# Optimization experiments

Measured on AMD Instinct MI355X. Metric: run time of the kernel, lower is better.

The kernel has to match this reference:

```python
import jax, jax.numpy as jnp
import numpy as np

ACT_BW = 8
PAR_BW = 4
EPS = 1e-8

def fake_quant(t, bw):
    # symmetric per-tensor fake quantization with dynamic absmax observer
    qmax = float(2 ** (bw - 1) - 1)
    scale = jnp.maximum(jnp.max(jnp.abs(t)) / qmax, EPS)
    q = jnp.clip(jnp.round(t / scale), -qmax, qmax) * scale
    # straight-through estimator (matches torch fake-quant backward)
    return t + jax.lax.stop_gradient(q - t)

def setup_inputs() -> dict:
    key = jax.random.key(0)
    k1, k2, k3 = jax.random.split(key, 3)
    tokens, d_in, d_out = 4096, 4096, 4096
    x = jax.random.normal(k1, (tokens, d_in), dtype=jnp.float32)
    # kaiming-uniform-ish init scale
    bound_w = 1.0 / np.sqrt(d_in)
    weight = jax.random.uniform(k2, (d_out, d_in), dtype=jnp.float32, minval=-bound_w, maxval=bound_w)
    b = jax.random.uniform(k3, (d_out,), dtype=jnp.float32, minval=-bound_w, maxval=bound_w)
    return {"x": x, "weight": weight, "b": b}

def reference(x, weight, b):
    # 1) requantize input activations (act_bitwidth)
    xq = fake_quant(x, ACT_BW)
    # 2) quantize weight (par_bitwidth), transpose [out,in] -> [in,out]
    wq = fake_quant(weight, PAR_BW).T
    # 3) quantize bias (act_bitwidth)
    bq = fake_quant(b, ACT_BW)
    # 4) AddMM: bias + x @ w^T, then requantize the output (multiplier's quantizer)
    out = bq + jnp.matmul(xq, wq)  # [tokens, out_features]
    return fake_quant(out, ACT_BW)
```

## Files before the change

kernel.cpp:

```cpp
#include <hip/hip_runtime.h>

#define NELEM (4096 * 4096)
#define KDIM 4096
#define NDIM 4096
#define DOUT 4096
#define EPSQ 1e-8f
#define STRIDE_MEM (2048 * 256)

typedef __attribute__((ext_vector_type(4))) int i32x4;

typedef __attribute__((address_space(3))) void lds_void;
typedef const __attribute__((address_space(1))) void gbl_void;

__device__ __forceinline__ void load_lds16(const void* g, void* l) {
    __builtin_amdgcn_global_load_lds((gbl_void*)g, (lds_void*)l, 16, 0, 0);
}

__device__ __forceinline__ float wave_max64(float v) {
#pragma unroll
    for (int off = 32; off > 0; off >>= 1)
        v = fmaxf(v, __shfl_down(v, off));
    return v;
}

__global__ __launch_bounds__(256) void absmax_xwb(
    const float4* __restrict__ x, const float4* __restrict__ w,
    const float* __restrict__ b, unsigned* __restrict__ amax)
{
    float mx = 0.f, mw = 0.f;
    int i = blockIdx.x * 256 + threadIdx.x;
#pragma unroll
    for (int it = 0; it < 8; ++it, i += STRIDE_MEM) {
        float4 a = x[i];
        float4 c = w[i];
        mx = fmaxf(mx, fmaxf(fmaxf(fabsf(a.x), fabsf(a.y)), fmaxf(fabsf(a.z), fabsf(a.w))));
        mw = fmaxf(mw, fmaxf(fmaxf(fabsf(c.x), fabsf(c.y)), fmaxf(fabsf(c.z), fabsf(c.w))));
    }
    float mb = 0.f;
    if (blockIdx.x == 0) {
#pragma unroll
        for (int t = 0; t < DOUT / 256; ++t)
            mb = fmaxf(mb, fabsf(b[t * 256 + threadIdx.x]));
    }

    mx = wave_max64(mx); mw = wave_max64(mw); mb = wave_max64(mb);
    __shared__ float red[3][4];
    const int wave = threadIdx.x >> 6, lane = threadIdx.x & 63;
    if (lane == 0) { red[0][wave] = mx; red[1][wave] = mw; red[2][wave] = mb; }
    __syncthreads();
    if (threadIdx.x == 0) {
        float r0 = fmaxf(fmaxf(red[0][0], red[0][1]), fmaxf(red[0][2], red[0][3]));
        float r1 = fmaxf(fmaxf(red[1][0], red[1][1]), fmaxf(red[1][2], red[1][3]));
        atomicMax(&amax[0], __float_as_uint(r0));
        atomicMax(&amax[1], __float_as_uint(r1));
        if (blockIdx.x == 0) {
            float r2 = fmaxf(fmaxf(red[2][0], red[2][1]), fmaxf(red[2][2], red[2][3]));
            atomicMax(&amax[2], __float_as_uint(r2));
        }
    }
}

__device__ __forceinline__ int pack4(float4 a, float s, float qmax) {
    int b0 = (int)fminf(fmaxf(rintf(a.x / s), -qmax), qmax);
    int b1 = (int)fminf(fmaxf(rintf(a.y / s), -qmax), qmax);
    int b2 = (int)fminf(fmaxf(rintf(a.z / s), -qmax), qmax);
    int b3 = (int)fminf(fmaxf(rintf(a.w / s), -qmax), qmax);
    return (b0 & 0xff) | ((b1 & 0xff) << 8) | ((b2 & 0xff) << 16) | (b3 << 24);
}

__global__ __launch_bounds__(256) void quant_xwb(
    const float4* __restrict__ x, const float4* __restrict__ w,
    const float* __restrict__ b, const unsigned* __restrict__ amax,
    int* __restrict__ qx, int* __restrict__ qw, float* __restrict__ bq)
{
    const float sx = fmaxf(__uint_as_float(amax[0]) / 127.0f, EPSQ);
    const float sw = fmaxf(__uint_as_float(amax[1]) / 7.0f, EPSQ);
    int i = blockIdx.x * 256 + threadIdx.x;
#pragma unroll
    for (int it = 0; it < 8; ++it, i += STRIDE_MEM) {
        qx[i] = pack4(x[i], sx, 127.f);
        qw[i] = pack4(w[i], sw, 7.f);
    }
    if (blockIdx.x == 0) {
        const float sb = fmaxf(__uint_as_float(amax[2]) / 127.0f, EPSQ);
#pragma unroll
        for (int t = 0; t < DOUT / 256; ++t) {
            int j = t * 256 + threadIdx.x;
            float q = fminf(fmaxf(rintf(b[j] / sb), -127.f), 127.f);
            bq[j] = q * sb;
        }
    }
}

__global__ __launch_bounds__(512, 2) void gemm_i8_8p(
    const char* __restrict__ qx,
    const char* __restrict__ qw,
    const float* __restrict__ bq,
    const unsigned* __restrict__ amax,
    float* __restrict__ out,
    unsigned* __restrict__ amax_out)
{
    constexpr int K = KDIM, N = NDIM;
    __shared__ char lds[131072];
    char* ldsA = lds;
    char* ldsB = lds + 65536;

    const int tid = threadIdx.x;
    const int wave = tid >> 6, lane = tid & 63;
    const int swz = (blockIdx.x & 7) * 32 + (blockIdx.x >> 3);
    const int bm = swz >> 4, bn = swz & 15;
    const int wm2 = wave >> 2;
    const int wn4 = wave & 3;

    const int sg16 = (((lane & 3) ^ ((lane >> 3) & 3)) << 4);
    const char* aG = qx + (size_t)(bm * 256 + wave * 16 + (lane >> 2)) * K + sg16;
    const char* bG = qw + (size_t)(bn * 256 + wave * 16 + (lane >> 2)) * K + sg16;

    const int frow = lane & 15;
    const int fks = (((lane >> 4) ^ ((frow >> 1) & 3)) << 4);
    const int aoff = (wm2 * 128 + frow) * 64 + fks;
    const int boff = (wn4 * 64 + frow) * 64 + fks;

    i32x4 acc[8][4] = {};

#define STAGE8(s) { const int p_ = (s) & 3;                                                  \
    load_lds16(aG + (size_t)(s) * 64,                  ldsA + p_ * 16384 + wave * 1024);     \
    load_lds16(aG + (size_t)128 * K + (size_t)(s) * 64, ldsA + p_ * 16384 + 8192 + wave * 1024); \
    load_lds16(bG + (size_t)(s) * 64,                  ldsB + p_ * 16384 + wave * 1024);     \
    load_lds16(bG + (size_t)128 * K + (size_t)(s) * 64, ldsB + p_ * 16384 + 8192 + wave * 1024); }

#define PHASE8(s, VMN, DO_ST) {                                                              \
    asm volatile("s_waitcnt vmcnt(%0)" :: "n"(VMN) : "memory");                              \
    __builtin_amdgcn_s_barrier();                                                            \
    __builtin_amdgcn_sched_barrier(0);                                                       \
    if (DO_ST) STAGE8((s) + 3);                                                              \
    const char* Ab = ldsA + ((s) & 3) * 16384 + aoff;                                        \
    const char* Bb = ldsB + ((s) & 3) * 16384 + boff;                                        \
    i32x4 af[8], bf[4];                                                                      \
    _Pragma("unroll") for (int mi = 0; mi < 8; ++mi)                                         \
        af[mi] = *(const i32x4*)(Ab + mi * 1024);                                            \
    _Pragma("unroll") for (int ni = 0; ni < 4; ++ni)                                         \
        bf[ni] = *(const i32x4*)(Bb + ni * 1024);                                            \
    __builtin_amdgcn_s_setprio(1);                                                           \
    _Pragma("unroll") for (int mi = 0; mi < 8; ++mi)                                         \
    _Pragma("unroll") for (int ni = 0; ni < 4; ++ni)                                         \
        acc[mi][ni] = __builtin_amdgcn_mfma_i32_16x16x64_i8(af[mi], bf[ni], acc[mi][ni], 0, 0, 0); \
    __builtin_amdgcn_s_setprio(0); }

    STAGE8(0); STAGE8(1); STAGE8(2);

    for (int s = 0; s < 61; ++s) PHASE8(s, 8, true);
    PHASE8(61, 8, false);
    PHASE8(62, 4, false);
    PHASE8(63, 0, false);

#undef PHASE8
#undef STAGE8

    const float sx = fmaxf(__uint_as_float(amax[0]) / 127.0f, EPSQ);
    const float sw = fmaxf(__uint_as_float(amax[1]) / 7.0f, EPSQ);
    const float s = sx * sw;
    const int col = lane & 15;
    const int rbase = (lane >> 4) * 4;
    float am = 0.f;
    float bqv[4];
#pragma unroll
    for (int ni = 0; ni < 4; ++ni) bqv[ni] = bq[bn * 256 + wn4 * 64 + ni * 16 + col];

#pragma unroll
    for (int mi = 0; mi < 8; ++mi) {
#pragma unroll
        for (int rr = 0; rr < 4; ++rr) {
            const int m = bm * 256 + wm2 * 128 + mi * 16 + rbase + rr;
            float* orow = out + (size_t)m * N + bn * 256 + wn4 * 64 + col;
#pragma unroll
            for (int ni = 0; ni < 4; ++ni) {
                float o = fmaf(s, (float)acc[mi][ni][rr], bqv[ni]);
                am = fmaxf(am, fabsf(o));
                orow[ni * 16] = o;
            }
        }
    }
    am = wave_max64(am);
    float* red = (float*)lds;
    if (lane == 0) red[wave] = am;
    __syncthreads();
    if (tid == 0) {
        float r = fmaxf(fmaxf(fmaxf(red[0], red[1]), fmaxf(red[2], red[3])),
                        fmaxf(fmaxf(red[4], red[5]), fmaxf(red[6], red[7])));
        atomicMax(amax_out, __float_as_uint(r));
    }
}

__global__ __launch_bounds__(256) void final_quant(
    float4* __restrict__ out, const unsigned* __restrict__ amax)
{
    const float so = fmaxf(__uint_as_float(amax[3]) / 127.0f, EPSQ);
    int i = blockIdx.x * 256 + threadIdx.x;
#pragma unroll
    for (int it = 0; it < 8; ++it, i += STRIDE_MEM) {
        float4 v = out[i];
        v.x = fminf(fmaxf(rintf(v.x / so), -127.f), 127.f) * so;
        v.y = fminf(fmaxf(rintf(v.y / so), -127.f), 127.f) * so;
        v.z = fminf(fmaxf(rintf(v.z / so), -127.f), 127.f) * so;
        v.w = fminf(fmaxf(rintf(v.w / so), -127.f), 127.f) * so;
        out[i] = v;
    }
}

extern "C" void kernel_launch(void* const* d_in, const int* in_sizes, int n_in,
                              void* d_out, int out_size, void* d_ws, size_t ws_size,
                              hipStream_t stream) {
    const float* x = (const float*)d_in[0];
    const float* w = (const float*)d_in[1];
    const float* b = (const float*)d_in[2];
    float* out = (float*)d_out;

    char* ws = (char*)d_ws;
    unsigned* amax = (unsigned*)ws;
    float* bq = (float*)(ws + 256);
    char* qx = (char*)(ws + 32768);
    char* qw = (char*)(ws + 32768 + (size_t)NELEM);

    hipMemsetAsync(amax, 0, 16, stream);
    hipLaunchKernelGGL(absmax_xwb, dim3(2048), dim3(256), 0, stream,
                       (const float4*)x, (const float4*)w, b, amax);
    hipLaunchKernelGGL(quant_xwb, dim3(2048), dim3(256), 0, stream,
                       (const float4*)x, (const float4*)w, b, amax,
                       (int*)qx, (int*)qw, bq);
    hipLaunchKernelGGL(gemm_i8_8p, dim3(256), dim3(512), 0, stream,
                       (const char*)qx, (const char*)qw, bq, amax, out, amax + 3);
    hipLaunchKernelGGL(final_quant, dim3(2048), dim3(256), 0, stream,
                       (float4*)out, amax);
}
```

Measured before the change: 280.4 us.

## Switch int8 GEMM to 32x32x32 MFMA and shard absmax atomics

```diff
diff --git a/kernel.cpp b/kernel.cpp
--- a/kernel.cpp
+++ b/kernel.cpp
@@ -8,6 +8,7 @@
 #define STRIDE_MEM (2048 * 256)
 
 typedef __attribute__((ext_vector_type(4))) int i32x4;
+typedef __attribute__((ext_vector_type(16))) int i32x16;
 
 typedef __attribute__((address_space(3))) void lds_void;
 typedef const __attribute__((address_space(1))) void gbl_void;
@@ -22,6 +23,7 @@
         v = fmaxf(v, __shfl_down(v, off));
     return v;
 }
+
 
 __global__ __launch_bounds__(256) void absmax_xwb(
     const float4* __restrict__ x, const float4* __restrict__ w,
@@ -51,13 +53,26 @@
     if (threadIdx.x == 0) {
         float r0 = fmaxf(fmaxf(red[0][0], red[0][1]), fmaxf(red[0][2], red[0][3]));
         float r1 = fmaxf(fmaxf(red[1][0], red[1][1]), fmaxf(red[1][2], red[1][3]));
-        atomicMax(&amax[0], __float_as_uint(r0));
-        atomicMax(&amax[1], __float_as_uint(r1));
+        const int sl = (blockIdx.x & 7) * 16;
+        atomicMax(&amax[sl], __float_as_uint(r0));
+        atomicMax(&amax[sl + 4], __float_as_uint(r1));
         if (blockIdx.x == 0) {
             float r2 = fmaxf(fmaxf(red[2][0], red[2][1]), fmaxf(red[2][2], red[2][3]));
-            atomicMax(&amax[2], __float_as_uint(r2));
+            atomicMax(&amax[128], __float_as_uint(r2));
         }
     }
+}
+
+__device__ __forceinline__ void load_scales(const unsigned* __restrict__ amax,
+                                            float& sx, float& sw) {
+    float sxm = 0.f, swm = 0.f;
+#pragma unroll
+    for (int j = 0; j < 8; ++j) {
+        sxm = fmaxf(sxm, __uint_as_float(amax[j * 16]));
+        swm = fmaxf(swm, __uint_as_float(amax[j * 16 + 4]));
+    }
+    sx = fmaxf(sxm / 127.0f, EPSQ);
+    sw = fmaxf(swm / 7.0f, EPSQ);
 }
 
 __device__ __forceinline__ int pack4(float4 a, float s, float qmax) {
@@ -73,8 +88,8 @@
     const float* __restrict__ b, const unsigned* __restrict__ amax,
     int* __restrict__ qx, int* __restrict__ qw, float* __restrict__ bq)
 {
-    const float sx = fmaxf(__uint_as_float(amax[0]) / 127.0f, EPSQ);
-    const float sw = fmaxf(__uint_as_float(amax[1]) / 7.0f, EPSQ);
+    float sx, sw;
+    load_scales(amax, sx, sw);
     int i = blockIdx.x * 256 + threadIdx.x;
 #pragma unroll
     for (int it = 0; it < 8; ++it, i += STRIDE_MEM) {
@@ -82,7 +97,7 @@
         qw[i] = pack4(w[i], sw, 7.f);
     }
     if (blockIdx.x == 0) {
-        const float sb = fmaxf(__uint_as_float(amax[2]) / 127.0f, EPSQ);
+        const float sb = fmaxf(__uint_as_float(amax[128]) / 127.0f, EPSQ);
 #pragma unroll
         for (int t = 0; t < DOUT / 256; ++t) {
             int j = t * 256 + threadIdx.x;
@@ -116,17 +131,18 @@
     const char* aG = qx + (size_t)(bm * 256 + wave * 16 + (lane >> 2)) * K + sg16;
     const char* bG = qw + (size_t)(bn * 256 + wave * 16 + (lane >> 2)) * K + sg16;
 
-    const int frow = lane & 15;
-    const int fks = (((lane >> 4) ^ ((frow >> 1) & 3)) << 4);
-    const int aoff = (wm2 * 128 + frow) * 64 + fks;
-    const int boff = (wn4 * 64 + frow) * 64 + fks;
-
-    i32x4 acc[8][4] = {};
+    const int l31 = lane & 31;
+    const int fks0 = ((((lane >> 5)) ^ ((lane >> 1) & 3)) << 4);
+    const int fks1 = ((((lane >> 5) | 2) ^ ((lane >> 1) & 3)) << 4);
+    const int aBase = wm2 * 8192 + l31 * 64;
+    const int bBase = (wn4 >> 1) * 8192 + (wn4 & 1) * 4096 + l31 * 64;
+
+    i32x16 acc[4][2] = {};
 
 #define STAGE8(s) { const int p_ = (s) & 3;                                                  \
-    load_lds16(aG + (size_t)(s) * 64,                  ldsA + p_ * 16384 + wave * 1024);     \
+    load_lds16(aG + (size_t)(s) * 64,                   ldsA + p_ * 16384 + wave * 1024);    \
     load_lds16(aG + (size_t)128 * K + (size_t)(s) * 64, ldsA + p_ * 16384 + 8192 + wave * 1024); \
-    load_lds16(bG + (size_t)(s) * 64,                  ldsB + p_ * 16384 + wave * 1024);     \
+    load_lds16(bG + (size_t)(s) * 64,                   ldsB + p_ * 16384 + wave * 1024);    \
     load_lds16(bG + (size_t)128 * K + (size_t)(s) * 64, ldsB + p_ * 16384 + 8192 + wave * 1024); }
 
 #define PHASE8(s, VMN, DO_ST) {                                                              \
@@ -134,17 +150,24 @@
     __builtin_amdgcn_s_barrier();                                                            \
     __builtin_amdgcn_sched_barrier(0);                                                       \
     if (DO_ST) STAGE8((s) + 3);                                                              \
-    const char* Ab = ldsA + ((s) & 3) * 16384 + aoff;                                        \
-    const char* Bb = ldsB + ((s) & 3) * 16384 + boff;                                        \
-    i32x4 af[8], bf[4];                                                                      \
-    _Pragma("unroll") for (int mi = 0; mi < 8; ++mi)                                         \
-        af[mi] = *(const i32x4*)(Ab + mi * 1024);                                            \
-    _Pragma("unroll") for (int ni = 0; ni < 4; ++ni)                                         \
-        bf[ni] = *(const i32x4*)(Bb + ni * 1024);                                            \
+    const char* Ab = ldsA + ((s) & 3) * 16384 + aBase;                                       \
+    const char* Bb = ldsB + ((s) & 3) * 16384 + bBase;                                       \
+    i32x4 a0[4], a1[4], b0[2], b1[2];                                                        \
+    _Pragma("unroll") for (int mi = 0; mi < 4; ++mi) {                                       \
+        a0[mi] = *(const i32x4*)(Ab + mi * 2048 + fks0);                                     \
+        a1[mi] = *(const i32x4*)(Ab + mi * 2048 + fks1);                                     \
+    }                                                                                        \
+    _Pragma("unroll") for (int ni = 0; ni < 2; ++ni) {                                       \
+        b0[ni] = *(const i32x4*)(Bb + ni * 2048 + fks0);                                     \
+        b1[ni] = *(const i32x4*)(Bb + ni * 2048 + fks1);                                     \
+    }                                                                                        \
     __builtin_amdgcn_s_setprio(1);                                                           \
-    _Pragma("unroll") for (int mi = 0; mi < 8; ++mi)                                         \
-    _Pragma("unroll") for (int ni = 0; ni < 4; ++ni)                                         \
-        acc[mi][ni] = __builtin_amdgcn_mfma_i32_16x16x64_i8(af[mi], bf[ni], acc[mi][ni], 0, 0, 0); \
+    _Pragma("unroll") for (int mi = 0; mi < 4; ++mi)                                         \
+    _Pragma("unroll") for (int ni = 0; ni < 2; ++ni)                                         \
+        acc[mi][ni] = __builtin_amdgcn_mfma_i32_32x32x32_i8(a0[mi], b0[ni], acc[mi][ni], 0, 0, 0); \
+    _Pragma("unroll") for (int mi = 0; mi < 4; ++mi)                                         \
+    _Pragma("unroll") for (int ni = 0; ni < 2; ++ni)                                         \
+        acc[mi][ni] = __builtin_amdgcn_mfma_i32_32x32x32_i8(a1[mi], b1[ni], acc[mi][ni], 0, 0, 0); \
     __builtin_amdgcn_s_setprio(0); }
 
     STAGE8(0); STAGE8(1); STAGE8(2);
@@ -157,27 +180,28 @@
 #undef PHASE8
 #undef STAGE8
 
-    const float sx = fmaxf(__uint_as_float(amax[0]) / 127.0f, EPSQ);
-    const float sw = fmaxf(__uint_as_float(amax[1]) / 7.0f, EPSQ);
+    float sx, sw;
+    load_scales(amax, sx, sw);
     const float s = sx * sw;
-    const int col = lane & 15;
-    const int rbase = (lane >> 4) * 4;
+    const int col = l31;
+    const int r4 = (lane >> 5) * 4;
     float am = 0.f;
-    float bqv[4];
-#pragma unroll
-    for (int ni = 0; ni < 4; ++ni) bqv[ni] = bq[bn * 256 + wn4 * 64 + ni * 16 + col];
-
-#pragma unroll
-    for (int mi = 0; mi < 8; ++mi) {
-#pragma unroll
-        for (int rr = 0; rr < 4; ++rr) {
-            const int m = bm * 256 + wm2 * 128 + mi * 16 + rbase + rr;
+    float bqv[2];
+#pragma unroll
+    for (int ni = 0; ni < 2; ++ni) bqv[ni] = bq[bn * 256 + wn4 * 64 + ni * 32 + col];
+
+#pragma unroll
+    for (int mi = 0; mi < 4; ++mi) {
+#pragma unroll
+        for (int reg = 0; reg < 16; ++reg) {
+            const int row = (reg & 3) + 8 * (reg >> 2) + r4;
+            const int m = bm * 256 + wm2 * 128 + mi * 32 + row;
             float* orow = out + (size_t)m * N + bn * 256 + wn4 * 64 + col;
 #pragma unroll
-            for (int ni = 0; ni < 4; ++ni) {
-                float o = fmaf(s, (float)acc[mi][ni][rr], bqv[ni]);
+            for (int ni = 0; ni < 2; ++ni) {
+                float o = fmaf(s, (float)acc[mi][ni][reg], bqv[ni]);
                 am = fmaxf(am, fabsf(o));
-                orow[ni * 16] = o;
+                orow[ni * 32] = o;
             }
         }
     }
@@ -193,9 +217,9 @@
 }
 
 __global__ __launch_bounds__(256) void final_quant(
-    float4* __restrict__ out, const unsigned* __restrict__ amax)
-{
-    const float so = fmaxf(__uint_as_float(amax[3]) / 127.0f, EPSQ);
+    float4* __restrict__ out, const unsigned* __restrict__ amax_out)
+{
+    const float so = fmaxf(__uint_as_float(amax_out[0]) / 127.0f, EPSQ);
     int i = blockIdx.x * 256 + threadIdx.x;
 #pragma unroll
     for (int it = 0; it < 8; ++it, i += STRIDE_MEM) {
@@ -218,18 +242,18 @@
 
     char* ws = (char*)d_ws;
     unsigned* amax = (unsigned*)ws;
-    float* bq = (float*)(ws + 256);
+    float* bq = (float*)(ws + 1024);
     char* qx = (char*)(ws + 32768);
     char* qw = (char*)(ws + 32768 + (size_t)NELEM);
 
-    hipMemsetAsync(amax, 0, 16, stream);
+    hipMemsetAsync(amax, 0, 1024, stream);
     hipLaunchKernelGGL(absmax_xwb, dim3(2048), dim3(256), 0, stream,
                        (const float4*)x, (const float4*)w, b, amax);
     hipLaunchKernelGGL(quant_xwb, dim3(2048), dim3(256), 0, stream,
                        (const float4*)x, (const float4*)w, b, amax,
                        (int*)qx, (int*)qw, bq);
     hipLaunchKernelGGL(gemm_i8_8p, dim3(256), dim3(512), 0, stream,
-                       (const char*)qx, (const char*)qw, bq, amax, out, amax + 3);
+                       (const char*)qx, (const char*)qw, bq, amax, out, amax + 132);
     hipLaunchKernelGGL(final_quant, dim3(2048), dim3(256), 0, stream,
-                       (float4*)out, amax);
-}
+                       (float4*)out, amax + 132);
+}
```

New measurement: 280.3 us. Within noise of the previous version (-0.1%).
